# Kernel optimization log

Hardware: AMD Instinct MI355X
Metric: run time of the kernel (lower is better)

Reference implementation:

```python
import jax, jax.numpy as jnp
import numpy as np

BS, NQ, NC = 64, 3000, 256
FH, FW, TOPK = 100, 100, 1500
INK_INF = jnp.float32(1e20)


def setup_inputs() -> dict:
    key = jax.random.key(0)
    k1, k2, k3 = jax.random.split(key, 3)
    u = jax.random.uniform(k1, (BS, NQ, 4), dtype=jnp.float32)
    # cx,cy in [0.25,0.75], w,h in [0,0.4] -> xyxy strictly inside [0,1]
    cxcy = 0.25 + 0.5 * u[..., :2]
    wh = 0.4 * u[..., 2:]
    output_coord = jnp.concatenate([cxcy, wh], axis=-1)
    output_class = jax.random.uniform(k2, (BS, NQ, NC), dtype=jnp.float32)
    # valid feature extent [valid_h, valid_w] per image (from ~mask cumsum in original)
    valid_feature_size = jax.random.randint(k3, (BS, 2), 50, FH + 1, dtype=jnp.int32)
    rows = jnp.arange(FH)[None, :, None]
    cols = jnp.arange(FW)[None, None, :]
    padding_mask = (rows >= valid_feature_size[:, 0][:, None, None]) | (
        cols >= valid_feature_size[:, 1][:, None, None]
    )  # (BS, FH, FW) bool, True = padded
    return {
        "output_coord": output_coord,
        "output_class": output_class,
        "valid_feature_size": valid_feature_size,
        "padding_mask": padding_mask,
        "feature_h": FH,
        "feature_w": FW,
        "topk": TOPK,
    }


def reference(output_coord, output_class, valid_feature_size, padding_mask,
              feature_h, feature_w, topk):
    bs = output_coord.shape[0]
    # scores = output_class.max(dim=-1); topk box select
    scores = jnp.max(output_class, axis=-1)                      # (bs, nq)
    _, topk_idx = jax.lax.top_k(scores, topk)                    # (bs, k)
    boxes = jnp.take_along_axis(output_coord, topk_idx[..., None], axis=1)  # (bs,k,4) cxcywh
    # box_cxcywh_to_xyxy
    cxcy, wh = boxes[..., :2], boxes[..., 2:]
    xyxy = jnp.concatenate([cxcy - 0.5 * wh, cxcy + 0.5 * wh], axis=-1)  # (bs,k,4)
    # valid_size.repeat(1,2) -> [vh, vw, vh, vw]
    vfs = valid_feature_size.astype(xyxy.dtype)
    scale = jnp.concatenate([vfs, vfs], axis=-1)[:, None, :]     # (bs,1,4)
    rng = jnp.floor(xyxy * scale).astype(jnp.int32)              # (bs,k,4)
    lx, ly, rx, ry = rng[..., 0], rng[..., 1], rng[..., 2], rng[..., 3]
    rows = jnp.arange(feature_h)
    cols = jnp.arange(feature_w)
    # per-box row/col membership; union over boxes via batched GEMM
    R = ((rows[None, None, :] >= ly[..., None]) & (rows[None, None, :] < ry[..., None])).astype(jnp.float32)  # (bs,k,h)
    C = ((cols[None, None, :] >= lx[..., None]) & (cols[None, None, :] < rx[..., None])).astype(jnp.float32)  # (bs,k,w)
    covered = jnp.einsum('bkh,bkw->bhw', R, C) > 0               # (bs,h,w)
    extra_mask = ~covered                                        # True outside every kept box
    # mask = extra_mask | padding_mask; float masked_fill(-INK_INF)
    full = extra_mask.reshape(bs, -1) | padding_mask.reshape(bs, -1)
    attn_mask = jnp.where(full, -INK_INF, jnp.float32(0.0))      # (bs, h*w)
    return attn_mask
```

## Files before the change

### kernel.cpp

```cpp
#include <hip/hip_runtime.h>

#define BS   64
#define NQ   3000
#define NC   256
#define FH   100
#define FW   100
#define TOPK 1500

__global__ __launch_bounds__(256) void scores_kernel(const float4* __restrict__ cls,
                                                     float* __restrict__ scores) {
    const int tid  = threadIdx.x;
    const int lane = tid & 63;
    const int wave = tid >> 6;
    const int row0 = blockIdx.x * 16 + wave * 4;
    const float4* p = cls + (size_t)row0 * (NC / 4) + lane;
    float4 a = p[0], b = p[64], c = p[128], d = p[192];
    float m0 = fmaxf(fmaxf(a.x, a.y), fmaxf(a.z, a.w));
    float m1 = fmaxf(fmaxf(b.x, b.y), fmaxf(b.z, b.w));
    float m2 = fmaxf(fmaxf(c.x, c.y), fmaxf(c.z, c.w));
    float m3 = fmaxf(fmaxf(d.x, d.y), fmaxf(d.z, d.w));
#pragma unroll
    for (int off = 32; off > 0; off >>= 1) {
        m0 = fmaxf(m0, __shfl_xor(m0, off, 64));
        m1 = fmaxf(m1, __shfl_xor(m1, off, 64));
        m2 = fmaxf(m2, __shfl_xor(m2, off, 64));
        m3 = fmaxf(m3, __shfl_xor(m3, off, 64));
    }
    if (lane < 4) {
        float m = (lane == 0) ? m0 : (lane == 1) ? m1 : (lane == 2) ? m2 : m3;
        scores[row0 + lane] = m;
    }
}

#define NSPLIT 8
#define NTM    512
#define QSLICE ((NQ + NSPLIT - 1) / NSPLIT)

__global__ __launch_bounds__(NTM) void raster_kernel(const float4* __restrict__ coord,
                                                     const int* __restrict__ vfs,
                                                     const float* __restrict__ scores,
                                                     unsigned* __restrict__ pcov) {
    __shared__ __align__(16) unsigned su[NQ];
    __shared__ int      hist[8][256];
    __shared__ unsigned cov[FH * 4];
    __shared__ int      eqlist[NQ];
    __shared__ int      wave_sum[4];
    __shared__ int      s_selbin, s_K, s_c24, s_qcut;

    const int part = blockIdx.x;
    const int b    = blockIdx.y;
    const int tid  = threadIdx.x;
    const int wid  = tid >> 6;

    {
        const uint4* sp = (const uint4*)(scores + b * NQ);
        uint4* sd = (uint4*)su;
        for (int i = tid; i < NQ / 4; i += NTM) sd[i] = sp[i];
    }
    for (int i = tid; i < FH * 4; i += NTM) cov[i] = 0u;
    if (tid == 0) s_c24 = 0;

    unsigned prefix = 0, pmask = 0;
    int K = TOPK;
#pragma unroll
    for (int p = 0; p < 4; ++p) {
        const int shift = 24 - 8 * p;
        for (int i = tid; i < 8 * 256; i += NTM) ((int*)hist)[i] = 0;
        __syncthreads();
        for (int q = tid; q < NQ; q += NTM) {
            unsigned u = su[q];
            if ((u & pmask) == prefix) {
                if (p == 3) eqlist[atomicAdd(&s_c24, 1)] = q;
                atomicAdd(&hist[wid][(u >> shift) & 0xFF], 1);
            }
        }
        __syncthreads();
        int x = 0, hx = 0, bin = 0;
        if (tid < 256) {
            bin = 255 - tid;
            hx = hist[0][bin] + hist[1][bin] + hist[2][bin] + hist[3][bin] +
                 hist[4][bin] + hist[5][bin] + hist[6][bin] + hist[7][bin];
            x = hx;
#pragma unroll
            for (int off = 1; off < 64; off <<= 1) {
                int y = __shfl_up(x, off, 64);
                if ((tid & 63) >= off) x += y;
            }
            if ((tid & 63) == 63) wave_sum[tid >> 6] = x;
        }
        __syncthreads();
        if (tid < 256) {
            int w = tid >> 6;
            for (int j = 0; j < w; ++j) x += wave_sum[j];
            int ge_incl = x;
            int ge_excl = x - hx;
            if (ge_incl >= K && ge_excl < K) {
                s_selbin = bin;
                s_K      = K - ge_excl;
            }
        }
        __syncthreads();
        prefix |= ((unsigned)s_selbin) << shift;
        pmask  |= (0xFFu << shift);
        K = s_K;
        __syncthreads();
    }
    const unsigned v      = prefix;
    const int      e_take = K;

    const int C24 = s_c24;
    for (int i = tid; i < C24; i += NTM) {
        int q = eqlist[i];
        if (su[q] == v) {
            int r = 0;
            for (int j = 0; j < C24; ++j) {
                int qj = eqlist[j];
                r += (su[qj] == v && qj < q) ? 1 : 0;
            }
            if (r == e_take - 1) s_qcut = q + 1;
        }
    }
    __syncthreads();
    const int qcut = s_qcut;

    const float s0 = (float)vfs[2 * b];
    const float s1 = (float)vfs[2 * b + 1];

    const int q0 = part * QSLICE;
    const int q1 = (q0 + QSLICE < NQ) ? (q0 + QSLICE) : NQ;
    for (int q = q0 + tid; q < q1; q += NTM) {
        unsigned u = su[q];
        if (u > v || (u == v && q < qcut)) {
            float4 c4 = coord[(size_t)b * NQ + q];
            float x1 = c4.x - 0.5f * c4.z, y1 = c4.y - 0.5f * c4.w;
            float x2 = c4.x + 0.5f * c4.z, y2 = c4.y + 0.5f * c4.w;
            int lx = (int)floorf(x1 * s0), ly = (int)floorf(y1 * s1);
            int rx = (int)floorf(x2 * s0), ry = (int)floorf(y2 * s1);
            int h0 = ly > 0 ? ly : 0, h1 = ry < FH ? ry : FH;
            int w0 = lx > 0 ? lx : 0, w1 = rx < FW ? rx : FW;
            if (h0 < h1 && w0 < w1) {
                unsigned m[4];
#pragma unroll
                for (int j = 0; j < 4; ++j) {
                    int lo = w0 - 32 * j; lo = lo < 0 ? 0 : lo;
                    int hi = w1 - 32 * j; hi = hi > 32 ? 32 : hi;
                    unsigned mm = 0u;
                    if (hi > lo) {
                        unsigned top = (hi >= 32) ? 0xFFFFFFFFu : ((1u << hi) - 1u);
                        unsigned bot = (lo <= 0) ? 0u : ((1u << lo) - 1u);
                        mm = top & ~bot;
                    }
                    m[j] = mm;
                }
                for (int h = h0; h < h1; ++h) {
#pragma unroll
                    for (int j = 0; j < 4; ++j)
                        if (m[j]) atomicOr(&cov[h * 4 + j], m[j]);
                }
            }
        }
    }
    __syncthreads();

    unsigned* dst = pcov + (size_t)(b * NSPLIT + part) * (FH * 4);
    for (int i = tid; i < FH * 4; i += NTM) dst[i] = cov[i];
}

__global__ __launch_bounds__(256) void emit_kernel(const unsigned* __restrict__ pcov,
                                                   const int* __restrict__ vfs,
                                                   float* __restrict__ out) {
    const int idx = blockIdx.x * 256 + threadIdx.x;
    if (idx >= BS * FH * (FW / 4)) return;
    const int b   = idx / (FH * (FW / 4));
    const int rem = idx - b * (FH * (FW / 4));
    const int h   = rem / (FW / 4);
    const int w4  = rem - h * (FW / 4);
    const int w   = w4 * 4;
    const unsigned* p = pcov + (size_t)b * NSPLIT * (FH * 4) + h * 4 + (w >> 5);
    unsigned acc = 0u;
#pragma unroll
    for (int s = 0; s < NSPLIT; ++s) acc |= p[s * (FH * 4)];
    const int  iv0  = vfs[2 * b], iv1 = vfs[2 * b + 1];
    const bool padr = (h >= iv0);
    float4 o;
    o.x = (((acc >> ((w + 0) & 31)) & 1u) && !(padr || (w + 0 >= iv1))) ? 0.0f : -1e20f;
    o.y = (((acc >> ((w + 1) & 31)) & 1u) && !(padr || (w + 1 >= iv1))) ? 0.0f : -1e20f;
    o.z = (((acc >> ((w + 2) & 31)) & 1u) && !(padr || (w + 2 >= iv1))) ? 0.0f : -1e20f;
    o.w = (((acc >> ((w + 3) & 31)) & 1u) && !(padr || (w + 3 >= iv1))) ? 0.0f : -1e20f;
    ((float4*)out)[idx] = o;
}

extern "C" void kernel_launch(void* const* d_in, const int* in_sizes, int n_in,
                              void* d_out, int out_size, void* d_ws, size_t ws_size,
                              hipStream_t stream) {
    const float4* coord = (const float4*)d_in[0];
    const float*  cls   = (const float*)d_in[1];
    const int*    vfs   = (const int*)d_in[2];
    float*    scores = (float*)d_ws;
    unsigned* pcov   = (unsigned*)((char*)d_ws + (size_t)BS * NQ * sizeof(float));
    float* out = (float*)d_out;

    const int rows = BS * NQ;
    scores_kernel<<<rows / 16, 256, 0, stream>>>((const float4*)cls, scores);
    raster_kernel<<<dim3(NSPLIT, BS), NTM, 0, stream>>>(coord, vfs, scores, pcov);
    const int emit_elems = BS * FH * (FW / 4);
    emit_kernel<<<(emit_elems + 255) / 256, 256, 0, stream>>>(pcov, vfs, out);
}
```

Measured before the change: 298.2 us.

## Fuse histogram build with score load, double-buffer hist, aggregate atomics per wave

The first radix-select histogram pass is folded into the global-to-shared score copy, and the histogram is double-buffered so the next buffer is cleared by idle threads during the scan. This removes two barriers per pass. Per-thread shared-memory atomics are replaced by wave-aggregated atomics (ballot, leader shuffle, popcount) to cut contention on hot bins. The aggregation loop can serialize when a wave holds many distinct bins, such as the high byte of uniform floats in the first pass.

```diff
diff --git a/kernel.cpp b/kernel.cpp
--- a/kernel.cpp
+++ b/kernel.cpp
@@ -32,6 +32,19 @@
     }
 }
 
+__device__ __forceinline__ void agg_add(int* __restrict__ hrow, unsigned bin, bool pr) {
+    unsigned long long act = __ballot(pr);
+    const int lane = threadIdx.x & 63;
+    while (act) {
+        const int leader = __ffsll((unsigned long long)act) - 1;
+        const unsigned lbin = (unsigned)__shfl((int)bin, leader, 64);
+        const unsigned long long same = __ballot(pr && (bin == lbin));
+        if (pr && (bin == lbin) && lane == leader)
+            atomicAdd(&hrow[lbin], (int)__popcll(same));
+        act &= ~same;
+    }
+}
+
 #define NSPLIT 8
 #define NTM    512
 #define QSLICE ((NQ + NSPLIT - 1) / NSPLIT)
@@ -41,7 +54,7 @@
                                                      const float* __restrict__ scores,
                                                      unsigned* __restrict__ pcov) {
     __shared__ __align__(16) unsigned su[NQ];
-    __shared__ int      hist[8][256];
+    __shared__ int      hist[2][8][256];
     __shared__ unsigned cov[FH * 4];
     __shared__ int      eqlist[NQ];
     __shared__ int      wave_sum[4];
@@ -52,34 +65,38 @@
     const int tid  = threadIdx.x;
     const int wid  = tid >> 6;
 
+    for (int i = tid; i < 8 * 256; i += NTM) ((int*)hist[0])[i] = 0;
+    for (int i = tid; i < FH * 4; i += NTM) cov[i] = 0u;
+    if (tid == 0) s_c24 = 0;
+    __syncthreads();
+
     {
         const uint4* sp = (const uint4*)(scores + b * NQ);
         uint4* sd = (uint4*)su;
-        for (int i = tid; i < NQ / 4; i += NTM) sd[i] = sp[i];
-    }
-    for (int i = tid; i < FH * 4; i += NTM) cov[i] = 0u;
-    if (tid == 0) s_c24 = 0;
+        int* hrow = hist[0][wid];
+        for (int i = tid; i < NQ / 4; i += NTM) {
+            uint4 v4 = sp[i];
+            sd[i] = v4;
+            agg_add(hrow, v4.x >> 24, true);
+            agg_add(hrow, v4.y >> 24, true);
+            agg_add(hrow, v4.z >> 24, true);
+            agg_add(hrow, v4.w >> 24, true);
+        }
+    }
+    __syncthreads();
 
     unsigned prefix = 0, pmask = 0;
     int K = TOPK;
 #pragma unroll
     for (int p = 0; p < 4; ++p) {
         const int shift = 24 - 8 * p;
-        for (int i = tid; i < 8 * 256; i += NTM) ((int*)hist)[i] = 0;
-        __syncthreads();
-        for (int q = tid; q < NQ; q += NTM) {
-            unsigned u = su[q];
-            if ((u & pmask) == prefix) {
-                if (p == 3) eqlist[atomicAdd(&s_c24, 1)] = q;
-                atomicAdd(&hist[wid][(u >> shift) & 0xFF], 1);
-            }
-        }
-        __syncthreads();
+        const int hb    = p & 1;
         int x = 0, hx = 0, bin = 0;
         if (tid < 256) {
             bin = 255 - tid;
-            hx = hist[0][bin] + hist[1][bin] + hist[2][bin] + hist[3][bin] +
-                 hist[4][bin] + hist[5][bin] + hist[6][bin] + hist[7][bin];
+            const int(*H)[256] = hist[hb];
+            hx = H[0][bin] + H[1][bin] + H[2][bin] + H[3][bin] +
+                 H[4][bin] + H[5][bin] + H[6][bin] + H[7][bin];
             x = hx;
 #pragma unroll
             for (int off = 1; off < 64; off <<= 1) {
@@ -87,6 +104,8 @@
                 if ((tid & 63) >= off) x += y;
             }
             if ((tid & 63) == 63) wave_sum[tid >> 6] = x;
+        } else if (p < 3) {
+            for (int i = tid - 256; i < 8 * 256; i += 256) ((int*)hist[hb ^ 1])[i] = 0;
         }
         __syncthreads();
         if (tid < 256) {
@@ -103,7 +122,16 @@
         prefix |= ((unsigned)s_selbin) << shift;
         pmask  |= (0xFFu << shift);
         K = s_K;
-        __syncthreads();
+        if (p < 3) {
+            const int nshift = 24 - 8 * (p + 1);
+            for (int q = tid; q < NQ; q += NTM) {
+                unsigned u  = su[q];
+                bool     pr = ((u & pmask) == prefix);
+                if (p == 2 && pr) eqlist[atomicAdd(&s_c24, 1)] = q;
+                agg_add(hist[hb ^ 1][wid], (u >> nshift) & 0xFF, pr);
+            }
+            __syncthreads();
+        }
     }
     const unsigned v      = prefix;
     const int      e_take = K;
```

Measured after the change: 321.6 us. 7.9% more time.
